# Kernel optimization log

Measured on AMD Instinct MI355X. Metric: run time of the kernel, lower is better.

The kernel has to match this reference:

```python
import jax, jax.numpy as jnp
import numpy as np

HIDDEN = 64

def setup_inputs() -> dict:
    key = jax.random.key(0)
    ks = jax.random.split(key, 10)
    B, E = 8, 200000
    h = jax.random.normal(ks[0], (B, E, HIDDEN), dtype=jnp.float32)
    J = jax.random.normal(ks[1], (B, E, 1), dtype=jnp.float32)
    b_in = jax.random.normal(ks[2], (B, E, 1), dtype=jnp.float32)
    b_out = jax.random.normal(ks[3], (B, E, 1), dtype=jnp.float32)
    d_in = HIDDEN + 4
    # PyTorch Linear default init: U(-1/sqrt(fan_in), 1/sqrt(fan_in))
    def lin(kw, kb, fan_in, fan_out):
        bound = 1.0 / np.sqrt(fan_in)
        W = jax.random.uniform(kw, (fan_in, fan_out), minval=-bound, maxval=bound, dtype=jnp.float32)
        b = jax.random.uniform(kb, (fan_out,), minval=-bound, maxval=bound, dtype=jnp.float32)
        return W, b
    W1, b1 = lin(ks[4], ks[5], d_in, 64)
    W2, b2 = lin(ks[6], ks[7], 64, 64)
    W3, b3 = lin(ks[8], ks[9], 64, 5)
    return {"h": h, "J": J, "b_in": b_in, "b_out": b_out,
            "W1": W1, "b1": b1, "W2": W2, "b2": b2, "W3": W3, "b3": b3}

def reference(h, J, b_in, b_out, W1, b1, W2, b2, W3, b3):
    # concat order matches torch.cat((h, b_in, b_out, J, -J), 2)
    x = jnp.concatenate((h, b_in, b_out, J, -J), axis=2)  # [B,E,hidden+4]
    x = jax.nn.relu(jnp.einsum('bei,io->beo', x, W1) + b1)
    x = jax.nn.relu(jnp.einsum('bei,io->beo', x, W2) + b2)
    message = jnp.einsum('bei,io->beo', x, W3) + b3  # [B,E,5]
    return message
```

## Files before the change

### kernel.cpp

```cpp
#include <hip/hip_runtime.h>

typedef __bf16 bf16x8 __attribute__((ext_vector_type(8)));
typedef float  f32x4  __attribute__((ext_vector_type(4)));

#define MFMA(A, B, C) __builtin_amdgcn_mfma_f32_16x16x32_bf16((A), (B), (C), 0, 0, 0)

#define B2_OFF 22528
#define B3_OFF 22784
__global__ __launch_bounds__(256, 5)
void msg_mlp(const float* __restrict__ hbuf, const float* __restrict__ Jbuf,
             const float* __restrict__ binb, const float* __restrict__ boutb,
             const float* __restrict__ W1, const float* __restrict__ b1,
             const float* __restrict__ W2, const float* __restrict__ b2,
             const float* __restrict__ W3, const float* __restrict__ b3,
             float* __restrict__ out, int n_rows, int n_tiles)
{
    __shared__ __align__(16) char wlds[22848];
    const int lane = threadIdx.x & 63;
    const int e = lane & 15;
    const int q = lane >> 4;
    const int wv = (int)(threadIdx.x >> 6);
    const int wid = blockIdx.x * 4 + wv;
    const int nw  = gridDim.x * 4;
    char* slot = wlds + lane * 16;

    if (wv == 0) {
#pragma unroll
      for (int mt = 0; mt < 4; ++mt)
#pragma unroll
        for (int kk = 0; kk < 2; ++kk) {
          bf16x8 v;
#pragma unroll
          for (int i = 0; i < 8; ++i)
            v[i] = (__bf16)W1[(16*q + 8*kk + i)*64 + 16*mt + e];
          *(bf16x8*)(slot + (mt*2 + kk) * 1024) = v;
        }
#pragma unroll
      for (int mt = 0; mt < 4; ++mt) {
        const int o = 16*mt + e;
        float w0;
        if      (q == 0) w0 =  W1[64*64 + o];
        else if (q == 1) w0 =  W1[65*64 + o];
        else if (q == 2) w0 =  W1[66*64 + o];
        else             w0 = -W1[67*64 + o];
        bf16x8 v;
        v[0] = (__bf16)w0;
        v[1] = (q == 0) ? (__bf16)b1[o] : (__bf16)0.0f;
#pragma unroll
        for (int i = 2; i < 8; ++i) v[i] = (__bf16)0.0f;
        *(bf16x8*)(slot + (8 + mt) * 1024) = v;
      }
    } else if (wv == 1) {
#pragma unroll
      for (int mt = 0; mt < 4; ++mt)
#pragma unroll
        for (int kk = 0; kk < 2; ++kk) {
          bf16x8 v;
#pragma unroll
          for (int i = 0; i < 8; ++i) {
            const int f = 16*(2*kk + (i>>2)) + 4*q + (i&3);
            v[i] = (__bf16)W2[f*64 + 16*mt + e];
          }
          *(bf16x8*)(slot + (12 + mt*2 + kk) * 1024) = v;
        }
    } else if (wv == 2) {
#pragma unroll
      for (int kk = 0; kk < 2; ++kk) {
        bf16x8 v;
#pragma unroll
        for (int i = 0; i < 8; ++i) {
          const int f = 16*(2*kk + (i>>2)) + 4*q + (i&3);
          v[i] = (e < 5) ? (__bf16)W3[f*5 + e] : (__bf16)0.0f;
        }
        *(bf16x8*)(slot + (20 + kk) * 1024) = v;
      }
      if (lane < 16)
        ((float*)(wlds + B3_OFF))[lane] = (lane < 5) ? b3[lane] : 0.0f;
    } else {
      ((float*)(wlds + B2_OFF))[lane] = b2[lane];
    }

    const float* sptr = (q == 0) ? binb : (q == 1) ? boutb : Jbuf;
    const __bf16 biasf = (q == 0) ? (__bf16)1.0f : (__bf16)0.0f;

    __syncthreads();

#pragma unroll 1
    for (int t = wid; t < n_tiles; t += nw) {
      int z0 = 0;
      asm volatile("" : "+s"(z0));
      const char* Wf = slot + z0;
      const char* Wb = wlds + 16*q + z0;

      int re = t * 16 + e;
      if (re >= n_rows) re = n_rows - 1;
      const float* hr = hbuf + (size_t)re * 64 + q * 16;
      const f32x4 v0 = *(const f32x4*)(hr);
      const f32x4 v1 = *(const f32x4*)(hr + 4);
      const f32x4 v2 = *(const f32x4*)(hr + 8);
      const f32x4 v3 = *(const f32x4*)(hr + 12);
      const float s  = sptr[re];

      bf16x8 xb0, xb1, xb2;
#pragma unroll
      for (int i = 0; i < 4; ++i) {
        xb0[i]     = (__bf16)v0[i];
        xb0[i + 4] = (__bf16)v1[i];
        xb1[i]     = (__bf16)v2[i];
        xb1[i + 4] = (__bf16)v3[i];
      }
      xb2[0] = (__bf16)s; xb2[1] = biasf;
#pragma unroll
      for (int i = 2; i < 8; ++i) xb2[i] = (__bf16)0.0f;

      f32x4 acc1[4];
#pragma unroll
      for (int mt = 0; mt < 4; ++mt) {
        const bf16x8 wa = *(const bf16x8*)(Wf + (mt*2 + 0) * 1024);
        const bf16x8 wb = *(const bf16x8*)(Wf + (mt*2 + 1) * 1024);
        const bf16x8 wx = *(const bf16x8*)(Wf + (8 + mt)  * 1024);
        acc1[mt] = (f32x4){0.f, 0.f, 0.f, 0.f};
        acc1[mt] = MFMA(wa, xb0, acc1[mt]);
        acc1[mt] = MFMA(wb, xb1, acc1[mt]);
        acc1[mt] = MFMA(wx, xb2, acc1[mt]);
      }
      bf16x8 y[2];
#pragma unroll
      for (int kk = 0; kk < 2; ++kk)
#pragma unroll
        for (int i = 0; i < 8; ++i)
          y[kk][i] = (__bf16)fmaxf(acc1[2*kk + (i>>2)][i & 3], 0.0f);

      f32x4 acc2[4];
#pragma unroll
      for (int mt = 0; mt < 4; ++mt) {
        const bf16x8 wa = *(const bf16x8*)(Wf + (12 + mt*2 + 0) * 1024);
        const bf16x8 wb = *(const bf16x8*)(Wf + (12 + mt*2 + 1) * 1024);
        acc2[mt] = *(const f32x4*)(Wb + B2_OFF + 64*mt);
        acc2[mt] = MFMA(wa, y[0], acc2[mt]);
        acc2[mt] = MFMA(wb, y[1], acc2[mt]);
      }
      bf16x8 z[2];
#pragma unroll
      for (int kk = 0; kk < 2; ++kk)
#pragma unroll
        for (int i = 0; i < 8; ++i)
          z[kk][i] = (__bf16)fmaxf(acc2[2*kk + (i>>2)][i & 3], 0.0f);

      f32x4 acc3 = *(const f32x4*)(Wb + B3_OFF);
      acc3 = MFMA(*(const bf16x8*)(Wf + 20 * 1024), z[0], acc3);
      acc3 = MFMA(*(const bf16x8*)(Wf + 21 * 1024), z[1], acc3);

      const int rowi = t * 16 + e;
      if (rowi < n_rows) {
        float* orow = out + (size_t)rowi * 5;
        if (q == 0) {
          orow[0] = acc3[0]; orow[1] = acc3[1];
          orow[2] = acc3[2]; orow[3] = acc3[3];
        } else if (q == 1) {
          orow[4] = acc3[0];
        }
      }
    }
}

extern "C" void kernel_launch(void* const* d_in, const int* in_sizes, int n_in,
                              void* d_out, int out_size, void* d_ws, size_t ws_size,
                              hipStream_t stream) {
    const float* h     = (const float*)d_in[0];
    const float* J     = (const float*)d_in[1];
    const float* b_in  = (const float*)d_in[2];
    const float* b_out = (const float*)d_in[3];
    const float* W1    = (const float*)d_in[4];
    const float* b1    = (const float*)d_in[5];
    const float* W2    = (const float*)d_in[6];
    const float* b2    = (const float*)d_in[7];
    const float* W3    = (const float*)d_in[8];
    const float* b3    = (const float*)d_in[9];
    float* out = (float*)d_out;

    const int n_rows  = in_sizes[1];
    const int n_tiles = (n_rows + 15) / 16;

    const int MAXW   = 5120;
    const int iters  = (n_tiles + MAXW - 1) / MAXW;
    const int waves  = (n_tiles + iters - 1) / iters;
    const int blocks = (waves + 3) / 4;

    dim3 grid(blocks), block(256);
    hipLaunchKernelGGL(msg_mlp, grid, block, 0, stream,
                       h, J, b_in, b_out, W1, b1, W2, b2, W3, b3,
                       out, n_rows, n_tiles);
}
```

Baseline: 95.30 us.

## Keep layer-2/3 weights in registers, use nontemporal IO, fixed grid

Layer-2 and layer-3 weight fragments are now loaded once into per-lane registers instead of being read from LDS in every tile iteration. This shrinks the LDS footprint to the W1 fragments and biases, and lowers the occupancy hint from 5 to 4 blocks to make room for the extra registers. Input loads and output stores switch to nontemporal builtins to cut cache pollution on the streaming data. The grid becomes a fixed 1024 blocks rather than being sized from the tile count, which changes how tiles are split across waves.

```diff
diff --git a/kernel.cpp b/kernel.cpp
--- a/kernel.cpp
+++ b/kernel.cpp
@@ -5,9 +5,9 @@
 
 #define MFMA(A, B, C) __builtin_amdgcn_mfma_f32_16x16x32_bf16((A), (B), (C), 0, 0, 0)
 
-#define B2_OFF 22528
-#define B3_OFF 22784
-__global__ __launch_bounds__(256, 5)
+#define B2_OFF 12288
+#define B3_OFF 12544
+__global__ __launch_bounds__(256, 4)
 void msg_mlp(const float* __restrict__ hbuf, const float* __restrict__ Jbuf,
              const float* __restrict__ binb, const float* __restrict__ boutb,
              const float* __restrict__ W1, const float* __restrict__ b1,
@@ -15,7 +15,7 @@
              const float* __restrict__ W3, const float* __restrict__ b3,
              float* __restrict__ out, int n_rows, int n_tiles)
 {
-    __shared__ __align__(16) char wlds[22848];
+    __shared__ __align__(16) char wlds[12608];
     const int lane = threadIdx.x & 63;
     const int e = lane & 15;
     const int q = lane >> 4;
@@ -35,6 +35,7 @@
             v[i] = (__bf16)W1[(16*q + 8*kk + i)*64 + 16*mt + e];
           *(bf16x8*)(slot + (mt*2 + kk) * 1024) = v;
         }
+    } else if (wv == 1) {
 #pragma unroll
       for (int mt = 0; mt < 4; ++mt) {
         const int o = 16*mt + e;
@@ -50,35 +51,31 @@
         for (int i = 2; i < 8; ++i) v[i] = (__bf16)0.0f;
         *(bf16x8*)(slot + (8 + mt) * 1024) = v;
       }
-    } else if (wv == 1) {
+    } else if (wv == 2) {
+      ((float*)(wlds + B2_OFF))[lane] = b2[lane];
+    } else {
+      if (lane < 16)
+        ((float*)(wlds + B3_OFF))[lane] = (lane < 5) ? b3[lane] : 0.0f;
+    }
+
+    bf16x8 a2[4][2];
 #pragma unroll
-      for (int mt = 0; mt < 4; ++mt)
+    for (int mt = 0; mt < 4; ++mt)
 #pragma unroll
-        for (int kk = 0; kk < 2; ++kk) {
-          bf16x8 v;
-#pragma unroll
-          for (int i = 0; i < 8; ++i) {
-            const int f = 16*(2*kk + (i>>2)) + 4*q + (i&3);
-            v[i] = (__bf16)W2[f*64 + 16*mt + e];
-          }
-          *(bf16x8*)(slot + (12 + mt*2 + kk) * 1024) = v;
-        }
-    } else if (wv == 2) {
-#pragma unroll
-      for (int kk = 0; kk < 2; ++kk) {
-        bf16x8 v;
+      for (int kk = 0; kk < 2; ++kk)
 #pragma unroll
         for (int i = 0; i < 8; ++i) {
           const int f = 16*(2*kk + (i>>2)) + 4*q + (i&3);
-          v[i] = (e < 5) ? (__bf16)W3[f*5 + e] : (__bf16)0.0f;
+          a2[mt][kk][i] = (__bf16)W2[f*64 + 16*mt + e];
         }
-        *(bf16x8*)(slot + (20 + kk) * 1024) = v;
+    bf16x8 a3[2];
+#pragma unroll
+    for (int kk = 0; kk < 2; ++kk)
+#pragma unroll
+      for (int i = 0; i < 8; ++i) {
+        const int f = 16*(2*kk + (i>>2)) + 4*q + (i&3);
+        a3[kk][i] = (e < 5) ? (__bf16)W3[f*5 + e] : (__bf16)0.0f;
       }
-      if (lane < 16)
-        ((float*)(wlds + B3_OFF))[lane] = (lane < 5) ? b3[lane] : 0.0f;
-    } else {
-      ((float*)(wlds + B2_OFF))[lane] = b2[lane];
-    }
 
     const float* sptr = (q == 0) ? binb : (q == 1) ? boutb : Jbuf;
     const __bf16 biasf = (q == 0) ? (__bf16)1.0f : (__bf16)0.0f;
@@ -95,11 +92,11 @@
       int re = t * 16 + e;
       if (re >= n_rows) re = n_rows - 1;
       const float* hr = hbuf + (size_t)re * 64 + q * 16;
-      const f32x4 v0 = *(const f32x4*)(hr);
-      const f32x4 v1 = *(const f32x4*)(hr + 4);
-      const f32x4 v2 = *(const f32x4*)(hr + 8);
-      const f32x4 v3 = *(const f32x4*)(hr + 12);
-      const float s  = sptr[re];
+      const f32x4 v0 = __builtin_nontemporal_load((const f32x4*)(hr));
+      const f32x4 v1 = __builtin_nontemporal_load((const f32x4*)(hr + 4));
+      const f32x4 v2 = __builtin_nontemporal_load((const f32x4*)(hr + 8));
+      const f32x4 v3 = __builtin_nontemporal_load((const f32x4*)(hr + 12));
+      const float s  = __builtin_nontemporal_load(sptr + re);
 
       bf16x8 xb0, xb1, xb2;
 #pragma unroll
@@ -134,11 +131,9 @@
       f32x4 acc2[4];
 #pragma unroll
       for (int mt = 0; mt < 4; ++mt) {
-        const bf16x8 wa = *(const bf16x8*)(Wf + (12 + mt*2 + 0) * 1024);
-        const bf16x8 wb = *(const bf16x8*)(Wf + (12 + mt*2 + 1) * 1024);
         acc2[mt] = *(const f32x4*)(Wb + B2_OFF + 64*mt);
-        acc2[mt] = MFMA(wa, y[0], acc2[mt]);
-        acc2[mt] = MFMA(wb, y[1], acc2[mt]);
+        acc2[mt] = MFMA(a2[mt][0], y[0], acc2[mt]);
+        acc2[mt] = MFMA(a2[mt][1], y[1], acc2[mt]);
       }
       bf16x8 z[2];
 #pragma unroll
@@ -148,17 +143,19 @@
           z[kk][i] = (__bf16)fmaxf(acc2[2*kk + (i>>2)][i & 3], 0.0f);
 
       f32x4 acc3 = *(const f32x4*)(Wb + B3_OFF);
-      acc3 = MFMA(*(const bf16x8*)(Wf + 20 * 1024), z[0], acc3);
-      acc3 = MFMA(*(const bf16x8*)(Wf + 21 * 1024), z[1], acc3);
+      acc3 = MFMA(a3[0], z[0], acc3);
+      acc3 = MFMA(a3[1], z[1], acc3);
 
       const int rowi = t * 16 + e;
       if (rowi < n_rows) {
         float* orow = out + (size_t)rowi * 5;
         if (q == 0) {
-          orow[0] = acc3[0]; orow[1] = acc3[1];
-          orow[2] = acc3[2]; orow[3] = acc3[3];
+          __builtin_nontemporal_store(acc3[0], orow + 0);
+          __builtin_nontemporal_store(acc3[1], orow + 1);
+          __builtin_nontemporal_store(acc3[2], orow + 2);
+          __builtin_nontemporal_store(acc3[3], orow + 3);
         } else if (q == 1) {
-          orow[4] = acc3[0];
+          __builtin_nontemporal_store(acc3[0], orow + 4);
         }
       }
     }
@@ -182,12 +179,7 @@
     const int n_rows  = in_sizes[1];
     const int n_tiles = (n_rows + 15) / 16;
 
-    const int MAXW   = 5120;
-    const int iters  = (n_tiles + MAXW - 1) / MAXW;
-    const int waves  = (n_tiles + iters - 1) / iters;
-    const int blocks = (waves + 3) / 4;
-
-    dim3 grid(blocks), block(256);
+    dim3 grid(1024), block(256);
     hipLaunchKernelGGL(msg_mlp, grid, block, 0, stream,
                        h, J, b_in, b_out, W1, b1, W2, b2, W3, b3,
                        out, n_rows, n_tiles);
```

Result: slower. 165.1 us (+73.2%).
